# Kernel tuning notes

Hardware: AMD Instinct MI355X
Metric: run time of the kernel (lower is better)

## Reference

```python
import jax, jax.numpy as jnp
import numpy as np

NB_HEAD = 8
SIZE_PER_HEAD = 64
MAX_LEN = 1024
D_IN = 512
BATCH = 8
NEG_BIG = 1e12  # matches the torch module's mask * 1000000000000.0


def setup_inputs() -> dict:
    key = jax.random.key(0)
    ks = jax.random.split(key, 6)
    return {
        "Q_seq": jax.random.normal(ks[0], (BATCH, MAX_LEN, D_IN), dtype=jnp.float32),
        "K_seq": jax.random.normal(ks[1], (BATCH, MAX_LEN, D_IN), dtype=jnp.float32),
        "V_seq": jax.random.normal(ks[2], (BATCH, MAX_LEN, D_IN), dtype=jnp.float32),
        "WQ": jax.random.normal(ks[3], (D_IN, NB_HEAD * SIZE_PER_HEAD), dtype=jnp.float32),
        "WK": jax.random.normal(ks[4], (D_IN, NB_HEAD * SIZE_PER_HEAD), dtype=jnp.float32),
        "WV": jax.random.normal(ks[5], (D_IN, NB_HEAD * SIZE_PER_HEAD), dtype=jnp.float32),
    }


def reference(Q_seq, K_seq, V_seq, WQ, WK, WV):
    B, L, _ = Q_seq.shape
    H, D = NB_HEAD, SIZE_PER_HEAD
    # QKV projections -> [B, H, L, D]
    q = (Q_seq @ WQ).reshape(B, L, H, D).transpose(0, 2, 1, 3)
    k = (K_seq @ WK).reshape(B, L, H, D).transpose(0, 2, 1, 3)
    v = (V_seq @ WV).reshape(B, L, H, D).transpose(0, 2, 1, 3)
    # scaled dot-product scores [B, H, Lq, Lk]
    scores = jnp.einsum("bhqd,bhkd->bhqk", q, k) / jnp.sqrt(jnp.float32(D))
    # causal mask: the torch Mask() subtracts 1e12 where key_idx > query_idx
    causal = jnp.triu(jnp.ones((L, L), dtype=scores.dtype), k=1)  # 1 where k > q
    scores = scores - causal[None, None, :, :] * NEG_BIG
    attn = jax.nn.softmax(scores, axis=-1)
    out = jnp.einsum("bhqk,bhkd->bhqd", attn, v)  # [B, H, L, D]
    return out.transpose(0, 2, 1, 3).reshape(B, L, H * D)
```

## Files before the change

kernel.cpp:

```cpp
#include <hip/hip_runtime.h>
#include <cstddef>

#define LEN    1024
#define DIN    512
#define NHEAD  8
#define HDIM   64
#define BATCH  8

typedef __attribute__((ext_vector_type(8))) short  short8;
typedef __attribute__((ext_vector_type(4))) float  f32x4;

#define MFMA16(a, b, c) __builtin_amdgcn_mfma_f32_16x16x32_bf16((a), (b), (c), 0, 0, 0)

__device__ __forceinline__ unsigned short bf_hi(float x) {
    unsigned u = __float_as_uint(x);
    return (unsigned short)((u + 0x7fffu + ((u >> 16) & 1u)) >> 16);
}
__device__ __forceinline__ void bf_split(float x, unsigned short& h, unsigned short& l) {
    unsigned u  = __float_as_uint(x);
    unsigned hu = (u + 0x7fffu + ((u >> 16) & 1u)) >> 16;
    h = (unsigned short)hu;
    l = bf_hi(x - __uint_as_float(hu << 16));
}

__global__ __launch_bounds__(256)
void wprep(const float* __restrict__ WQ, const float* __restrict__ WK,
           const float* __restrict__ WV, unsigned short* __restrict__ wt)
{
    __shared__ float T[64][68];
    const int z = blockIdx.z;
    const float* W = (z == 0) ? WQ : (z == 1) ? WK : WV;
    unsigned short* Wth = wt + (size_t)z * 524288;
    unsigned short* Wtl = Wth + 262144;
    const int k0 = blockIdx.x * 64, n0 = blockIdx.y * 64;
    const int t = threadIdx.x;
    #pragma unroll
    for (int e = 0; e < 4; ++e) {
        int f = e * 256 + t, r = f >> 4, c4 = (f & 15) << 2;
        *(float4*)&T[r][c4] = *(const float4*)&W[(size_t)(k0 + r) * 512 + n0 + c4];
    }
    __syncthreads();
    #pragma unroll
    for (int e = 0; e < 4; ++e) {
        int f = e * 256 + t, nr = f >> 4, kc4 = (f & 15) << 2;
        ushort4 h, l;
        bf_split(T[kc4 + 0][nr], h.x, l.x);
        bf_split(T[kc4 + 1][nr], h.y, l.y);
        bf_split(T[kc4 + 2][nr], h.z, l.z);
        bf_split(T[kc4 + 3][nr], h.w, l.w);
        *(ushort4*)&Wth[(size_t)(n0 + nr) * 512 + k0 + kc4] = h;
        *(ushort4*)&Wtl[(size_t)(n0 + nr) * 512 + k0 + kc4] = l;
    }
}

#define PSTR 40

__global__ __launch_bounds__(256)
void proj_mfma(const float* __restrict__ Qin, const float* __restrict__ Kin,
               const float* __restrict__ Vin, const unsigned short* __restrict__ wt,
               unsigned short* __restrict__ qh, unsigned short* __restrict__ ql,
               unsigned short* __restrict__ kh, unsigned short* __restrict__ kl,
               unsigned short* __restrict__ vh)
{
    __shared__ unsigned short Ah[128 * PSTR], Al[128 * PSTR],
                              Bh[128 * PSTR], Bl[128 * PSTR];
    const int z = blockIdx.z;
    const float* X = (z == 0) ? Qin : (z == 1) ? Kin : Vin;
    unsigned short* oh = (z == 0) ? qh : (z == 1) ? kh : vh;
    unsigned short* ol = (z == 0) ? ql : kl;
    const unsigned short* Wth = wt + (size_t)z * 524288;
    const unsigned short* Wtl = Wth + 262144;

    const int t = threadIdx.x, lane = t & 63, w = t >> 6;
    const int wm = w & 1, wn = w >> 1;
    const int m0 = blockIdx.x * 128, n0 = blockIdx.y * 128;
    const int lm = lane & 15, lq = lane >> 4;
    const int ar = t >> 1, ak = (t & 1) * 16;

    const float* Xp = X + (size_t)(m0 + ar) * 512 + ak;
    const unsigned short* Bph = Wth + (size_t)(n0 + ar) * 512 + ak;
    const unsigned short* Bpl = Wtl + (size_t)(n0 + ar) * 512 + ak;

    f32x4 acc[4][4];
    #pragma unroll
    for (int i = 0; i < 4; ++i)
        #pragma unroll
        for (int j = 0; j < 4; ++j) acc[i][j] = 0.f;

    for (int k0 = 0; k0 < 512; k0 += 32) {
        float4 av[4];
        #pragma unroll
        for (int e = 0; e < 4; ++e) av[e] = *(const float4*)(Xp + k0 + e * 4);
        uint4 b0 = *(const uint4*)(Bph + k0);
        uint4 b1 = *(const uint4*)(Bph + k0 + 8);
        uint4 b2 = *(const uint4*)(Bpl + k0);
        uint4 b3 = *(const uint4*)(Bpl + k0 + 8);
        __syncthreads();
        #pragma unroll
        for (int e = 0; e < 4; ++e) {
            ushort4 h, l;
            bf_split(av[e].x, h.x, l.x);
            bf_split(av[e].y, h.y, l.y);
            bf_split(av[e].z, h.z, l.z);
            bf_split(av[e].w, h.w, l.w);
            *(ushort4*)&Ah[ar * PSTR + ak + e * 4] = h;
            *(ushort4*)&Al[ar * PSTR + ak + e * 4] = l;
        }
        *(uint4*)&Bh[ar * PSTR + ak]     = b0;
        *(uint4*)&Bh[ar * PSTR + ak + 8] = b1;
        *(uint4*)&Bl[ar * PSTR + ak]     = b2;
        *(uint4*)&Bl[ar * PSTR + ak + 8] = b3;
        __syncthreads();

        short8 a_h[4], a_l[4];
        #pragma unroll
        for (int mi = 0; mi < 4; ++mi) {
            int off = (wm * 64 + mi * 16 + lm) * PSTR + lq * 8;
            a_h[mi] = *(const short8*)&Ah[off];
            a_l[mi] = *(const short8*)&Al[off];
        }
        #pragma unroll
        for (int ni = 0; ni < 4; ++ni) {
            int off = (wn * 64 + ni * 16 + lm) * PSTR + lq * 8;
            short8 b_h = *(const short8*)&Bh[off];
            short8 b_l = *(const short8*)&Bl[off];
            #pragma unroll
            for (int mi = 0; mi < 4; ++mi) {
                acc[mi][ni] = MFMA16(a_l[mi], b_h, acc[mi][ni]);
                acc[mi][ni] = MFMA16(a_h[mi], b_l, acc[mi][ni]);
                acc[mi][ni] = MFMA16(a_h[mi], b_h, acc[mi][ni]);
            }
        }
    }

    const float sc = (z == 0) ? 0.125f : 1.0f;
    #pragma unroll
    for (int mi = 0; mi < 4; ++mi)
        #pragma unroll
        for (int ni = 0; ni < 4; ++ni) {
            int n_abs = n0 + wn * 64 + ni * 16 + lm;
            int hd = n_abs >> 6, d = n_abs & 63;
            #pragma unroll
            for (int r = 0; r < 4; ++r) {
                int m_abs = m0 + wm * 64 + mi * 16 + lq * 4 + r;
                int b = m_abs >> 10, li = m_abs & 1023;
                size_t idx = (((size_t)b * NHEAD + hd) * LEN + li) * HDIM + d;
                unsigned short hv, lv;
                bf_split(acc[mi][ni][r] * sc, hv, lv);
                oh[idx] = hv;
                if (z < 2) ol[idx] = lv;
            }
        }
}

__global__ __launch_bounds__(256)
void attn_mfma(const unsigned short* __restrict__ qh, const unsigned short* __restrict__ ql,
               const unsigned short* __restrict__ kh, const unsigned short* __restrict__ kl,
               const unsigned short* __restrict__ vh, float* __restrict__ out)
{
    __shared__ unsigned short sm[23040];
    unsigned short* Kh  = sm;
    unsigned short* Kl  = sm + 4608;
    unsigned short* Vt  = sm + 9216;
    unsigned short* Pb  = sm + 13824;
    unsigned short* Qsh = sm;
    unsigned short* Qsl = sm + 9216;

    const int t = threadIdx.x, lane = t & 63, w = t >> 6;
    const int lm = lane & 15, lq = lane >> 4;
    const int qt = (int)gridDim.x - 1 - (int)blockIdx.x;
    const int bh = blockIdx.y;
    const size_t base = (size_t)bh * LEN * HDIM;
    const unsigned short* qhb = qh + base;
    const unsigned short* qlb = ql + base;
    const unsigned short* khb = kh + base;
    const unsigned short* klb = kl + base;
    const unsigned short* vhb = vh + base;
    const int Q0  = qt * 128;
    const int Q0w = Q0 + w * 32;

    #pragma unroll
    for (int e = 0; e < 4; ++e) {
        int f = e * 256 + t, r = f >> 3, s8 = (f & 7) * 8;
        *(uint4*)&Qsh[r * 72 + s8] = *(const uint4*)&qhb[(size_t)(Q0 + r) * 64 + s8];
        *(uint4*)&Qsl[r * 72 + s8] = *(const uint4*)&qlb[(size_t)(Q0 + r) * 64 + s8];
    }
    __syncthreads();
    short8 qfh[2][2], qfl[2][2];
    #pragma unroll
    for (int mi = 0; mi < 2; ++mi)
        #pragma unroll
        for (int ks = 0; ks < 2; ++ks) {
            int off = (w * 32 + mi * 16 + lm) * 72 + ks * 32 + lq * 8;
            qfh[mi][ks] = *(const short8*)&Qsh[off];
            qfl[mi][ks] = *(const short8*)&Qsl[off];
        }

    float m_i[2][4], l_i[2][4];
    f32x4 oacc[2][4];
    #pragma unroll
    for (int mi = 0; mi < 2; ++mi)
        #pragma unroll
        for (int r = 0; r < 4; ++r) { m_i[mi][r] = -1e30f; l_i[mi][r] = 0.f; }
    #pragma unroll
    for (int mi = 0; mi < 2; ++mi)
        #pragma unroll
        for (int nd = 0; nd < 4; ++nd) oacc[mi][nd] = 0.f;

    const int jend = 2 * qt + 1;
    for (int jb = 0; jb <= jend; ++jb) {
        __syncthreads();
        #pragma unroll
        for (int e = 0; e < 2; ++e) {
            int f = e * 256 + t, r = f >> 3, s8 = (f & 7) * 8;
            *(uint4*)&Kh[r * 72 + s8] = *(const uint4*)&khb[(size_t)(jb * 64 + r) * 64 + s8];
            *(uint4*)&Kl[r * 72 + s8] = *(const uint4*)&klb[(size_t)(jb * 64 + r) * 64 + s8];
        }
        {
            int key = t & 63, g0 = t >> 6;
            #pragma unroll
            for (int e = 0; e < 4; ++e) {
                int g = g0 + e * 4;
                ushort4 vv = *(const ushort4*)&vhb[(size_t)(jb * 64 + key) * 64 + g * 4];
                Vt[(g * 4 + 0) * 72 + key] = vv.x;
                Vt[(g * 4 + 1) * 72 + key] = vv.y;
                Vt[(g * 4 + 2) * 72 + key] = vv.z;
                Vt[(g * 4 + 3) * 72 + key] = vv.w;
            }
        }
        __syncthreads();

        const bool active = (jb * 64 <= Q0w + 31);
        if (active) {
            f32x4 sf[2][4];
            #pragma unroll
            for (int mi = 0; mi < 2; ++mi)
                #pragma unroll
                for (int ni = 0; ni < 4; ++ni) sf[mi][ni] = 0.f;
            #pragma unroll
            for (int ks = 0; ks < 2; ++ks)
                #pragma unroll
                for (int ni = 0; ni < 4; ++ni) {
                    int off = (ni * 16 + lm) * 72 + ks * 32 + lq * 8;
                    short8 b_h = *(const short8*)&Kh[off];
                    short8 b_l = *(const short8*)&Kl[off];
                    #pragma unroll
                    for (int mi = 0; mi < 2; ++mi) {
                        sf[mi][ni] = MFMA16(qfl[mi][ks], b_h, sf[mi][ni]);
                        sf[mi][ni] = MFMA16(qfh[mi][ks], b_l, sf[mi][ni]);
                        sf[mi][ni] = MFMA16(qfh[mi][ks], b_h, sf[mi][ni]);
                    }
                }
            if (jb * 64 + 63 > Q0w) {
                #pragma unroll
                for (int mi = 0; mi < 2; ++mi)
                    #pragma unroll
                    for (int ni = 0; ni < 4; ++ni) {
                        int key = jb * 64 + ni * 16 + lm;
                        #pragma unroll
                        for (int r = 0; r < 4; ++r) {
                            int qi = Q0w + mi * 16 + lq * 4 + r;
                            if (key > qi) sf[mi][ni][r] = -1e30f;
                        }
                    }
            }
            #pragma unroll
            for (int mi = 0; mi < 2; ++mi)
                #pragma unroll
                for (int r = 0; r < 4; ++r) {
                    float mv = fmaxf(fmaxf(sf[mi][0][r], sf[mi][1][r]),
                                     fmaxf(sf[mi][2][r], sf[mi][3][r]));
                    mv = fmaxf(mv, __shfl_xor(mv, 1));
                    mv = fmaxf(mv, __shfl_xor(mv, 2));
                    mv = fmaxf(mv, __shfl_xor(mv, 4));
                    mv = fmaxf(mv, __shfl_xor(mv, 8));
                    float mo = m_i[mi][r];
                    float mn = fmaxf(mo, mv);
                    float al = __expf(mo - mn);
                    m_i[mi][r] = mn;
                    float rs = 0.f;
                    int prow = (w * 32 + mi * 16 + lq * 4 + r) * 72 + lm;
                    #pragma unroll
                    for (int ni = 0; ni < 4; ++ni) {
                        float p = __expf(sf[mi][ni][r] - mn);
                        rs += p;
                        Pb[prow + ni * 16] = bf_hi(p);
                    }
                    rs += __shfl_xor(rs, 1);
                    rs += __shfl_xor(rs, 2);
                    rs += __shfl_xor(rs, 4);
                    rs += __shfl_xor(rs, 8);
                    l_i[mi][r] = l_i[mi][r] * al + rs;
                    #pragma unroll
                    for (int nd = 0; nd < 4; ++nd) oacc[mi][nd][r] *= al;
                }
        }
        __syncthreads();
        if (active) {
            short8 pf[2][2];
            #pragma unroll
            for (int mi = 0; mi < 2; ++mi)
                #pragma unroll
                for (int ks = 0; ks < 2; ++ks)
                    pf[mi][ks] = *(const short8*)&Pb[(w * 32 + mi * 16 + lm) * 72 + ks * 32 + lq * 8];
            #pragma unroll
            for (int ks = 0; ks < 2; ++ks)
                #pragma unroll
                for (int nd = 0; nd < 4; ++nd) {
                    short8 vf = *(const short8*)&Vt[(nd * 16 + lm) * 72 + ks * 32 + lq * 8];
                    #pragma unroll
                    for (int mi = 0; mi < 2; ++mi)
                        oacc[mi][nd] = MFMA16(pf[mi][ks], vf, oacc[mi][nd]);
                }
        }
    }

    const int b = bh >> 3, hd = bh & 7;
    #pragma unroll
    for (int mi = 0; mi < 2; ++mi)
        #pragma unroll
        for (int r = 0; r < 4; ++r) {
            int qrow = Q0w + mi * 16 + lq * 4 + r;
            float inv = 1.0f / l_i[mi][r];
            #pragma unroll
            for (int nd = 0; nd < 4; ++nd) {
                int d = nd * 16 + lm;
                out[((size_t)b * LEN + qrow) * (NHEAD * HDIM) + hd * 64 + d] =
                    oacc[mi][nd][r] * inv;
            }
        }
}

extern "C" void kernel_launch(void* const* d_in, const int* in_sizes, int n_in,
                              void* d_out, int out_size, void* d_ws, size_t ws_size,
                              hipStream_t stream)
{
    const float* Qin = (const float*)d_in[0];
    const float* Kin = (const float*)d_in[1];
    const float* Vin = (const float*)d_in[2];
    const float* WQ  = (const float*)d_in[3];
    const float* WK  = (const float*)d_in[4];
    const float* WV  = (const float*)d_in[5];

    unsigned short* ws = (unsigned short*)d_ws;
    const size_t per = (size_t)BATCH * NHEAD * LEN * HDIM;
    unsigned short* qh = ws;
    unsigned short* ql = ws + per;
    unsigned short* kh = ws + 2 * per;
    unsigned short* kl = ws + 3 * per;
    unsigned short* vh = ws + 4 * per;
    unsigned short* wt = ws + 5 * per;

    wprep    <<<dim3(8, 8, 3),  256, 0, stream>>>(WQ, WK, WV, wt);
    proj_mfma<<<dim3(64, 4, 3), 256, 0, stream>>>(Qin, Kin, Vin, wt, qh, ql, kh, kl, vh);
    attn_mfma<<<dim3(8, 64),    256, 0, stream>>>(qh, ql, kh, kl, vh, (float*)d_out);
}
```

Before: 225.8 us.

## Prefetch tiles, pack Q/K hi-lo, pre-transpose V, use DPP reductions and exp2

The projection kernel now prefetches the next k-slice into registers while computing the current one. It also stores Q/K hi/lo bf16 pairs packed into 32-bit words, and writes V already transposed so attention can copy it with vector stores instead of scalar scatter. Attention register-prefetches the next K/V tile, replaces shuffle reductions with DPP row operations, folds log2(e) into the Q scale to use exp2, and drops one barrier between softmax and the PV MMA. The grid is flattened so all heads of the longest causal tiles are scheduled first, at the cost of extra register pressure.

```diff
diff --git a/kernel.cpp b/kernel.cpp
--- a/kernel.cpp
+++ b/kernel.cpp
@@ -21,6 +21,32 @@
     unsigned hu = (u + 0x7fffu + ((u >> 16) & 1u)) >> 16;
     h = (unsigned short)hu;
     l = bf_hi(x - __uint_as_float(hu << 16));
+}
+__device__ __forceinline__ void unpack4(uint4 u, ushort4& h, ushort4& l) {
+    h = make_ushort4((unsigned short)(u.x >> 16), (unsigned short)(u.y >> 16),
+                     (unsigned short)(u.z >> 16), (unsigned short)(u.w >> 16));
+    l = make_ushort4((unsigned short)(u.x & 0xffff), (unsigned short)(u.y & 0xffff),
+                     (unsigned short)(u.z & 0xffff), (unsigned short)(u.w & 0xffff));
+}
+
+template<int CTRL>
+__device__ __forceinline__ float dpp_mov(float x) {
+    return __int_as_float(__builtin_amdgcn_update_dpp(
+        0, __float_as_int(x), CTRL, 0xF, 0xF, true));
+}
+__device__ __forceinline__ float red16_max(float x) {
+    x = fmaxf(x, dpp_mov<0xB1>(x));
+    x = fmaxf(x, dpp_mov<0x4E>(x));
+    x = fmaxf(x, dpp_mov<0x141>(x));
+    x = fmaxf(x, dpp_mov<0x140>(x));
+    return x;
+}
+__device__ __forceinline__ float red16_sum(float x) {
+    x += dpp_mov<0xB1>(x);
+    x += dpp_mov<0x4E>(x);
+    x += dpp_mov<0x141>(x);
+    x += dpp_mov<0x140>(x);
+    return x;
 }
 
 __global__ __launch_bounds__(256)
@@ -58,16 +84,13 @@
 __global__ __launch_bounds__(256)
 void proj_mfma(const float* __restrict__ Qin, const float* __restrict__ Kin,
                const float* __restrict__ Vin, const unsigned short* __restrict__ wt,
-               unsigned short* __restrict__ qh, unsigned short* __restrict__ ql,
-               unsigned short* __restrict__ kh, unsigned short* __restrict__ kl,
+               unsigned int* __restrict__ qhl, unsigned int* __restrict__ khl,
                unsigned short* __restrict__ vh)
 {
     __shared__ unsigned short Ah[128 * PSTR], Al[128 * PSTR],
                               Bh[128 * PSTR], Bl[128 * PSTR];
     const int z = blockIdx.z;
     const float* X = (z == 0) ? Qin : (z == 1) ? Kin : Vin;
-    unsigned short* oh = (z == 0) ? qh : (z == 1) ? kh : vh;
-    unsigned short* ol = (z == 0) ? ql : kl;
     const unsigned short* Wth = wt + (size_t)z * 524288;
     const unsigned short* Wtl = Wth + 262144;
 
@@ -87,14 +110,16 @@
         #pragma unroll
         for (int j = 0; j < 4; ++j) acc[i][j] = 0.f;
 
+    float4 av[4];
+    uint4 b0, b1, b2, b3;
+    #pragma unroll
+    for (int e = 0; e < 4; ++e) av[e] = *(const float4*)(Xp + e * 4);
+    b0 = *(const uint4*)(Bph);
+    b1 = *(const uint4*)(Bph + 8);
+    b2 = *(const uint4*)(Bpl);
+    b3 = *(const uint4*)(Bpl + 8);
+
     for (int k0 = 0; k0 < 512; k0 += 32) {
-        float4 av[4];
-        #pragma unroll
-        for (int e = 0; e < 4; ++e) av[e] = *(const float4*)(Xp + k0 + e * 4);
-        uint4 b0 = *(const uint4*)(Bph + k0);
-        uint4 b1 = *(const uint4*)(Bph + k0 + 8);
-        uint4 b2 = *(const uint4*)(Bpl + k0);
-        uint4 b3 = *(const uint4*)(Bpl + k0 + 8);
         __syncthreads();
         #pragma unroll
         for (int e = 0; e < 4; ++e) {
@@ -112,6 +137,15 @@
         *(uint4*)&Bl[ar * PSTR + ak + 8] = b3;
         __syncthreads();
 
+        if (k0 + 32 < 512) {
+            #pragma unroll
+            for (int e = 0; e < 4; ++e) av[e] = *(const float4*)(Xp + k0 + 32 + e * 4);
+            b0 = *(const uint4*)(Bph + k0 + 32);
+            b1 = *(const uint4*)(Bph + k0 + 40);
+            b2 = *(const uint4*)(Bpl + k0 + 32);
+            b3 = *(const uint4*)(Bpl + k0 + 40);
+        }
+
         short8 a_h[4], a_l[4];
         #pragma unroll
         for (int mi = 0; mi < 4; ++mi) {
@@ -133,30 +167,45 @@
         }
     }
 
-    const float sc = (z == 0) ? 0.125f : 1.0f;
-    #pragma unroll
-    for (int mi = 0; mi < 4; ++mi)
-        #pragma unroll
-        for (int ni = 0; ni < 4; ++ni) {
-            int n_abs = n0 + wn * 64 + ni * 16 + lm;
-            int hd = n_abs >> 6, d = n_abs & 63;
-            #pragma unroll
-            for (int r = 0; r < 4; ++r) {
-                int m_abs = m0 + wm * 64 + mi * 16 + lq * 4 + r;
-                int b = m_abs >> 10, li = m_abs & 1023;
-                size_t idx = (((size_t)b * NHEAD + hd) * LEN + li) * HDIM + d;
-                unsigned short hv, lv;
-                bf_split(acc[mi][ni][r] * sc, hv, lv);
-                oh[idx] = hv;
-                if (z < 2) ol[idx] = lv;
+    if (z < 2) {
+        unsigned int* o = (z == 0) ? qhl : khl;
+        const float sc = (z == 0) ? 0.18033688011112042f : 1.0f;
+        #pragma unroll
+        for (int mi = 0; mi < 4; ++mi)
+            #pragma unroll
+            for (int ni = 0; ni < 4; ++ni) {
+                int n_abs = n0 + wn * 64 + ni * 16 + lm;
+                int hd = n_abs >> 6, d = n_abs & 63;
+                #pragma unroll
+                for (int r = 0; r < 4; ++r) {
+                    int m_abs = m0 + wm * 64 + mi * 16 + lq * 4 + r;
+                    int b = m_abs >> 10, li = m_abs & 1023;
+                    unsigned short hv, lv;
+                    bf_split(acc[mi][ni][r] * sc, hv, lv);
+                    o[(((size_t)b * NHEAD + hd) * LEN + li) * HDIM + d] =
+                        ((unsigned)hv << 16) | lv;
+                }
             }
-        }
+    } else {
+        #pragma unroll
+        for (int mi = 0; mi < 4; ++mi) {
+            int m_base = m0 + wm * 64 + mi * 16 + lq * 4;
+            int b = m_base >> 10, l0 = m_base & 1023;
+            #pragma unroll
+            for (int ni = 0; ni < 4; ++ni) {
+                int n_abs = n0 + wn * 64 + ni * 16 + lm;
+                int hd = n_abs >> 6, d = n_abs & 63;
+                ushort4 hv = make_ushort4(bf_hi(acc[mi][ni][0]), bf_hi(acc[mi][ni][1]),
+                                          bf_hi(acc[mi][ni][2]), bf_hi(acc[mi][ni][3]));
+                *(ushort4*)&vh[(((size_t)b * NHEAD + hd) * HDIM + d) * LEN + l0] = hv;
+            }
+        }
+    }
 }
 
 __global__ __launch_bounds__(256)
-void attn_mfma(const unsigned short* __restrict__ qh, const unsigned short* __restrict__ ql,
-               const unsigned short* __restrict__ kh, const unsigned short* __restrict__ kl,
-               const unsigned short* __restrict__ vh, float* __restrict__ out)
+void attn_mfma(const unsigned int* __restrict__ qhl, const unsigned int* __restrict__ khl,
+               const unsigned short* __restrict__ vth, float* __restrict__ out)
 {
     __shared__ unsigned short sm[23040];
     unsigned short* Kh  = sm;
@@ -168,22 +217,24 @@
 
     const int t = threadIdx.x, lane = t & 63, w = t >> 6;
     const int lm = lane & 15, lq = lane >> 4;
-    const int qt = (int)gridDim.x - 1 - (int)blockIdx.x;
-    const int bh = blockIdx.y;
+    const int bx = blockIdx.x;
+    const int qt = 7 - (bx >> 6);
+    const int bh = bx & 63;
     const size_t base = (size_t)bh * LEN * HDIM;
-    const unsigned short* qhb = qh + base;
-    const unsigned short* qlb = ql + base;
-    const unsigned short* khb = kh + base;
-    const unsigned short* klb = kl + base;
-    const unsigned short* vhb = vh + base;
+    const unsigned int*   qb = qhl + base;
+    const unsigned int*   kb = khl + base;
+    const unsigned short* vb = vth + base;
     const int Q0  = qt * 128;
     const int Q0w = Q0 + w * 32;
 
     #pragma unroll
-    for (int e = 0; e < 4; ++e) {
-        int f = e * 256 + t, r = f >> 3, s8 = (f & 7) * 8;
-        *(uint4*)&Qsh[r * 72 + s8] = *(const uint4*)&qhb[(size_t)(Q0 + r) * 64 + s8];
-        *(uint4*)&Qsl[r * 72 + s8] = *(const uint4*)&qlb[(size_t)(Q0 + r) * 64 + s8];
+    for (int e = 0; e < 8; ++e) {
+        int f = e * 256 + t, r = f >> 4, c4 = (f & 15) << 2;
+        uint4 u = *(const uint4*)&qb[(size_t)(Q0 + r) * 64 + c4];
+        ushort4 h, l;
+        unpack4(u, h, l);
+        *(ushort4*)&Qsh[r * 72 + c4] = h;
+        *(ushort4*)&Qsl[r * 72 + c4] = l;
     }
     __syncthreads();
     short8 qfh[2][2], qfl[2][2];
@@ -207,28 +258,41 @@
         #pragma unroll
         for (int nd = 0; nd < 4; ++nd) oacc[mi][nd] = 0.f;
 
+    const int kr_ = t >> 4, kc4 = (t & 15) << 2;
+    const int vd_ = t >> 3, vs8 = (t & 7) << 3;
+
+    uint4 kreg[4], vreg[2];
+    #pragma unroll
+    for (int e = 0; e < 4; ++e)
+        kreg[e] = *(const uint4*)&kb[(size_t)(e * 16 + kr_) * 64 + kc4];
+    #pragma unroll
+    for (int e = 0; e < 2; ++e)
+        vreg[e] = *(const uint4*)&vb[(size_t)(e * 32 + vd_) * LEN + vs8];
+
     const int jend = 2 * qt + 1;
     for (int jb = 0; jb <= jend; ++jb) {
         __syncthreads();
         #pragma unroll
-        for (int e = 0; e < 2; ++e) {
-            int f = e * 256 + t, r = f >> 3, s8 = (f & 7) * 8;
-            *(uint4*)&Kh[r * 72 + s8] = *(const uint4*)&khb[(size_t)(jb * 64 + r) * 64 + s8];
-            *(uint4*)&Kl[r * 72 + s8] = *(const uint4*)&klb[(size_t)(jb * 64 + r) * 64 + s8];
-        }
-        {
-            int key = t & 63, g0 = t >> 6;
-            #pragma unroll
-            for (int e = 0; e < 4; ++e) {
-                int g = g0 + e * 4;
-                ushort4 vv = *(const ushort4*)&vhb[(size_t)(jb * 64 + key) * 64 + g * 4];
-                Vt[(g * 4 + 0) * 72 + key] = vv.x;
-                Vt[(g * 4 + 1) * 72 + key] = vv.y;
-                Vt[(g * 4 + 2) * 72 + key] = vv.z;
-                Vt[(g * 4 + 3) * 72 + key] = vv.w;
-            }
-        }
+        for (int e = 0; e < 4; ++e) {
+            int r = e * 16 + kr_;
+            ushort4 h, l;
+            unpack4(kreg[e], h, l);
+            *(ushort4*)&Kh[r * 72 + kc4] = h;
+            *(ushort4*)&Kl[r * 72 + kc4] = l;
+        }
+        #pragma unroll
+        for (int e = 0; e < 2; ++e)
+            *(uint4*)&Vt[(e * 32 + vd_) * 72 + vs8] = vreg[e];
         __syncthreads();
+
+        if (jb < jend) {
+            #pragma unroll
+            for (int e = 0; e < 4; ++e)
+                kreg[e] = *(const uint4*)&kb[(size_t)((jb + 1) * 64 + e * 16 + kr_) * 64 + kc4];
+            #pragma unroll
+            for (int e = 0; e < 2; ++e)
+                vreg[e] = *(const uint4*)&vb[(size_t)(e * 32 + vd_) * LEN + (jb + 1) * 64 + vs8];
+        }
 
         const bool active = (jb * 64 <= Q0w + 31);
         if (active) {
@@ -270,33 +334,24 @@
                 for (int r = 0; r < 4; ++r) {
                     float mv = fmaxf(fmaxf(sf[mi][0][r], sf[mi][1][r]),
                                      fmaxf(sf[mi][2][r], sf[mi][3][r]));
-                    mv = fmaxf(mv, __shfl_xor(mv, 1));
-                    mv = fmaxf(mv, __shfl_xor(mv, 2));
-                    mv = fmaxf(mv, __shfl_xor(mv, 4));
-                    mv = fmaxf(mv, __shfl_xor(mv, 8));
+                    mv = red16_max(mv);
                     float mo = m_i[mi][r];
                     float mn = fmaxf(mo, mv);
-                    float al = __expf(mo - mn);
+                    float al = __builtin_amdgcn_exp2f(mo - mn);
                     m_i[mi][r] = mn;
                     float rs = 0.f;
                     int prow = (w * 32 + mi * 16 + lq * 4 + r) * 72 + lm;
                     #pragma unroll
                     for (int ni = 0; ni < 4; ++ni) {
-                        float p = __expf(sf[mi][ni][r] - mn);
+                        float p = __builtin_amdgcn_exp2f(sf[mi][ni][r] - mn);
                         rs += p;
                         Pb[prow + ni * 16] = bf_hi(p);
                     }
-                    rs += __shfl_xor(rs, 1);
-                    rs += __shfl_xor(rs, 2);
-                    rs += __shfl_xor(rs, 4);
-                    rs += __shfl_xor(rs, 8);
+                    rs = red16_sum(rs);
                     l_i[mi][r] = l_i[mi][r] * al + rs;
                     #pragma unroll
                     for (int nd = 0; nd < 4; ++nd) oacc[mi][nd][r] *= al;
                 }
-        }
-        __syncthreads();
-        if (active) {
             short8 pf[2][2];
             #pragma unroll
             for (int mi = 0; mi < 2; ++mi)
@@ -342,16 +397,13 @@
     const float* WK  = (const float*)d_in[4];
     const float* WV  = (const float*)d_in[5];
 
-    unsigned short* ws = (unsigned short*)d_ws;
     const size_t per = (size_t)BATCH * NHEAD * LEN * HDIM;
-    unsigned short* qh = ws;
-    unsigned short* ql = ws + per;
-    unsigned short* kh = ws + 2 * per;
-    unsigned short* kl = ws + 3 * per;
-    unsigned short* vh = ws + 4 * per;
-    unsigned short* wt = ws + 5 * per;
+    unsigned int*   qhl = (unsigned int*)d_ws;
+    unsigned int*   khl = qhl + per;
+    unsigned short* vh  = (unsigned short*)(khl + per);
+    unsigned short* wt  = vh + per;
 
     wprep    <<<dim3(8, 8, 3),  256, 0, stream>>>(WQ, WK, WV, wt);
-    proj_mfma<<<dim3(64, 4, 3), 256, 0, stream>>>(Qin, Kin, Vin, wt, qh, ql, kh, kl, vh);
-    attn_mfma<<<dim3(8, 64),    256, 0, stream>>>(qh, ql, kh, kl, vh, (float*)d_out);
-}
+    proj_mfma<<<dim3(64, 4, 3), 256, 0, stream>>>(Qin, Kin, Vin, wt, qhl, khl, vh);
+    attn_mfma<<<dim3(512),      256, 0, stream>>>(qhl, khl, vh, (float*)d_out);
+}
```

New measurement: 202.1 us. 10.5% less time.
